# Kernel optimization log

Hardware: AMD Instinct MI355X
Metric: run time of the kernel (lower is better)

## Reference

```python
import jax, jax.numpy as jnp
import numpy as np

B, S, P, D, H = 2, 2048, 2048, 2048, 16
HD = D // H  # head_dim = 128


def setup_inputs() -> dict:
    key = jax.random.key(0)
    ks = jax.random.split(key, 8)
    scale = 1.0 / np.sqrt(D)
    return {
        "x": jax.random.normal(ks[0], (B, S, D), jnp.float32),
        "cache_k": jax.random.normal(ks[1], (B, P, D), jnp.float32),
        "cache_v": jax.random.normal(ks[2], (B, P, D), jnp.float32),
        "wq": jax.random.normal(ks[3], (D, D), jnp.float32) * scale,
        "bq": jnp.zeros((D,), jnp.float32),
        "wk": jax.random.normal(ks[4], (D, D), jnp.float32) * scale,
        "bk": jnp.zeros((D,), jnp.float32),
        "wv": jax.random.normal(ks[5], (D, D), jnp.float32) * scale,
        "bv": jnp.zeros((D,), jnp.float32),
        "wo": jax.random.normal(ks[6], (D, D), jnp.float32) * scale,
        "bo": jnp.zeros((D,), jnp.float32),
    }


def reference(x, cache_k, cache_v, wq, bq, wk, bk, wv, bv, wo, bo):
    bsz, seq_len, _ = x.shape
    q = x @ wq + bq                      # [B,S,D]
    k_new = x @ wk + bk                  # [B,S,D]
    v_new = x @ wv + bv
    # use_cache=True path: prepend cached (detached) keys/values
    k = jnp.concatenate([cache_k, k_new], axis=1)  # [B,P+S,D]
    v = jnp.concatenate([cache_v, v_new], axis=1)
    # split heads: [B,H,S,hd] / [B,H,K,hd]
    q = q.reshape(bsz, seq_len, H, HD).transpose(0, 2, 1, 3)
    k = k.reshape(bsz, -1, H, HD).transpose(0, 2, 1, 3)
    v = v.reshape(bsz, -1, H, HD).transpose(0, 2, 1, 3)
    scores = jnp.einsum("bhsd,bhkd->bhsk", q, k) / jnp.sqrt(jnp.float32(HD))
    attn = jax.nn.softmax(scores, axis=-1)          # full-softmax, no mask
    out = jnp.einsum("bhsk,bhkd->bhsd", attn, v)
    out = out.transpose(0, 2, 1, 3).reshape(bsz, seq_len, D)
    return out @ wo + bo
```

## Files before the change

### kernel.cpp

```cpp
#include <hip/hip_runtime.h>

typedef __attribute__((ext_vector_type(8))) short short8;
typedef __attribute__((ext_vector_type(4))) short short4_;
typedef __attribute__((ext_vector_type(4))) float f32x4;

#define AS1 __attribute__((address_space(1)))
#define AS3 __attribute__((address_space(3)))
#define GLD16(g, l) __builtin_amdgcn_global_load_lds((const AS1 void*)(g), (AS3 void*)(l), 16, 0, 0)

#define C2 0.12751743f

__device__ __forceinline__ unsigned short f2bf(float f) {
  unsigned int u = __float_as_uint(f);
  u += 0x7fffu + ((u >> 16) & 1u);
  return (unsigned short)(u >> 16);
}

__global__ __launch_bounds__(256) void k_transpose_w(
    const float* __restrict__ wq, const float* __restrict__ wk,
    const float* __restrict__ wv, const float* __restrict__ wo,
    unsigned short* __restrict__ wqkvT, unsigned short* __restrict__ woT)
{
  __shared__ float tile[64][65];
  const int z = blockIdx.z;
  const float* src = (z == 0) ? wq : (z == 1) ? wk : (z == 2) ? wv : wo;
  unsigned short* dst = (z == 3) ? woT : (wqkvT + (size_t)z * 2048 * 2048);
  const int k0 = blockIdx.y * 64, n0 = blockIdx.x * 64;
  const int tid = threadIdx.x;
#pragma unroll
  for (int p = 0; p < 4; ++p) {
    const int r = p * 16 + (tid >> 4);
    const int c = (tid & 15) * 4;
    f32x4 v = *(const f32x4*)(src + (size_t)(k0 + r) * 2048 + n0 + c);
    tile[r][c + 0] = v[0]; tile[r][c + 1] = v[1];
    tile[r][c + 2] = v[2]; tile[r][c + 3] = v[3];
  }
  __syncthreads();
#pragma unroll
  for (int p = 0; p < 2; ++p) {
    const int task = tid + p * 256;
    const int n = task >> 3;
    const int kc = (task & 7) * 8;
    short8 ov;
#pragma unroll
    for (int j = 0; j < 8; ++j) ov[j] = (short)f2bf(tile[kc + j][n]);
    *(short8*)(dst + (size_t)(n0 + n) * 2048 + k0 + kc) = ov;
  }
}

__global__ __launch_bounds__(256) void k_convert(
    const float* __restrict__ x, const float* __restrict__ ck, const float* __restrict__ cv,
    unsigned short* __restrict__ xbf, unsigned short* __restrict__ kfull,
    unsigned short* __restrict__ vfull)
{
  const int z = blockIdx.y;
  const size_t idx = ((size_t)blockIdx.x * 256 + threadIdx.x) * 8;
  const float* src = (z == 0) ? x : (z == 1) ? ck : cv;
  f32x4 a = *(const f32x4*)(src + idx);
  f32x4 b = *(const f32x4*)(src + idx + 4);
  short8 ov;
#pragma unroll
  for (int j = 0; j < 4; ++j) { ov[j] = (short)f2bf(a[j]); ov[j + 4] = (short)f2bf(b[j]); }
  unsigned short* dp; size_t di;
  if (z == 0) { dp = xbf; di = idx; }
  else {
    const size_t r = idx >> 11, cl = idx & 2047;
    const size_t orow = r + (r & ~(size_t)2047);
    di = orow * 2048 + cl;
    dp = (z == 1) ? kfull : vfull;
  }
  *(short8*)(dp + di) = ov;
}

template <int MODE>
__global__ __launch_bounds__(256, 2) void k_gemm(
    const unsigned short* __restrict__ A, const unsigned short* __restrict__ BT,
    unsigned short* __restrict__ Oq, unsigned short* __restrict__ Ok,
    unsigned short* __restrict__ Ov, float* __restrict__ Of,
    const float* __restrict__ b0, const float* __restrict__ b1,
    const float* __restrict__ b2, int K)
{
  __shared__ unsigned short Ah[128 * 32];
  __shared__ unsigned short Bh[128 * 32];
  const int tid = threadIdx.x;
  const int l = tid & 63, w = tid >> 6;
  const int l15 = l & 15, g = l >> 4;
  const int wr = (w >> 1) * 64, wc = (w & 1) * 64;
  const int bm = blockIdx.y, bn = blockIdx.x;
  const unsigned short* Ab = A + (size_t)bm * 128 * K;
  const unsigned short* Bb = BT + (size_t)bn * 128 * K;
  const int srow = l >> 2;
  const int scol = (l & 3) * 8;
  f32x4 acc[4][4];
#pragma unroll
  for (int i = 0; i < 4; ++i)
#pragma unroll
    for (int j = 0; j < 4; ++j)
#pragma unroll
      for (int e = 0; e < 4; ++e) acc[i][j][e] = 0.f;

  for (int kt = 0; kt < K; kt += 32) {
#pragma unroll
    for (int cc = 0; cc < 2; ++cc) {
      const int c = w + cc * 4;
      GLD16(Ab + (size_t)(c * 16 + srow) * K + kt + scol, &Ah[c * 512]);
      GLD16(Bb + (size_t)(c * 16 + srow) * K + kt + scol, &Bh[c * 512]);
    }
    __syncthreads();
    short8 af[4], bf[4];
#pragma unroll
    for (int i = 0; i < 4; ++i) {
      af[i] = *(const short8*)&Ah[(wr + i * 16 + l15) * 32 + g * 8];
      bf[i] = *(const short8*)&Bh[(wc + i * 16 + l15) * 32 + g * 8];
    }
#pragma unroll
    for (int i = 0; i < 4; ++i)
#pragma unroll
      for (int j = 0; j < 4; ++j)
        acc[i][j] = __builtin_amdgcn_mfma_f32_16x16x32_bf16(af[i], bf[j], acc[i][j], 0, 0, 0);
    __syncthreads();
  }

  const int rbase = bm * 128 + wr + g * 4;
  if (MODE == 0) {
    const int nglob = bn * 128;
    const int which = nglob >> 11;
    const int ncol0 = nglob & 2047;
    unsigned short* dst = (which == 0) ? Oq : (which == 1) ? Ok : Ov;
    const float* bias = (which == 0) ? b0 : (which == 1) ? b1 : b2;
#pragma unroll
    for (int j = 0; j < 4; ++j) {
      const int cc = ncol0 + wc + j * 16 + l15;
      const float bb = bias[cc];
#pragma unroll
      for (int i = 0; i < 4; ++i) {
#pragma unroll
        for (int ii = 0; ii < 4; ++ii) {
          const int rr = rbase + i * 16 + ii;
          const size_t orow = (which == 0) ? (size_t)rr
                                           : (size_t)(rr + (rr & ~2047) + 2048);
          dst[orow * 2048 + cc] = f2bf(acc[i][j][ii] + bb);
        }
      }
    }
  } else {
#pragma unroll
    for (int j = 0; j < 4; ++j) {
      const int cc = bn * 128 + wc + j * 16 + l15;
      const float bb = b0[cc];
#pragma unroll
      for (int i = 0; i < 4; ++i) {
#pragma unroll
        for (int ii = 0; ii < 4; ++ii) {
          const int rr = rbase + i * 16 + ii;
          Of[(size_t)rr * 2048 + cc] = acc[i][j][ii] + bb;
        }
      }
    }
  }
}

__global__ __launch_bounds__(256, 2) void k_flash(
    const unsigned short* __restrict__ qbuf, const unsigned short* __restrict__ kfull,
    const unsigned short* __restrict__ vfull, unsigned short* __restrict__ attnout)
{
  __shared__ char smem[65536];
  const int tid = threadIdx.x;
  const int l = tid & 63, w = tid >> 6;
  const int l15 = l & 15, g = l >> 4;
  const int qt = blockIdx.x, bh = blockIdx.y;
  const int b = bh >> 4, h = bh & 15;

  short8 qfA[4], qfB[4];
  {
    const int qrowA = qt * 128 + w * 32 + l15;
    const unsigned short* qpA = qbuf + ((size_t)(b * 2048 + qrowA)) * 2048 + h * 128 + g * 8;
    const unsigned short* qpB = qpA + 16 * 2048;
#pragma unroll
    for (int kk = 0; kk < 4; ++kk) {
      qfA[kk] = *(const short8*)(qpA + kk * 32);
      qfB[kk] = *(const short8*)(qpB + kk * 32);
    }
  }
  f32x4 oA[8], oB[8];
#pragma unroll
  for (int d = 0; d < 8; ++d)
#pragma unroll
    for (int e = 0; e < 4; ++e) { oA[d][e] = 0.f; oB[d][e] = 0.f; }
  float mA = -1e30f, mB = -1e30f, lsA = 0.f, lsB = 0.f;

  const unsigned short* kbase = kfull + ((size_t)b * 4096) * 2048 + h * 128;
  const unsigned short* vbase = vfull + ((size_t)b * 4096) * 2048 + h * 128;

  const int vg4 = tid & 15;
  const int vdc = tid >> 4;
  const int vcol4 = (vg4 & 8) | ((vg4 & 3) << 1) | ((vg4 >> 2) & 1);
  const int vu = vcol4 >> 1;
  const int vhalf = (vcol4 & 1) * 8;
  const int ksrow = l >> 4, ksu = l & 15;

  auto STAGEK = [&](int t, char* Kn) {
    const unsigned short* kb = kbase + (size_t)t * 64 * 2048;
#pragma unroll
    for (int ci = 0; ci < 4; ++ci) {
      const int c = w * 4 + ci;
      const int row = c * 4 + ksrow;
      GLD16(kb + (size_t)row * 2048 + ((ksu ^ (row & 7)) * 8), Kn + c * 1024);
    }
  };
  auto VLOAD = [&](int t, short8* r) {
    const unsigned short* vp = vbase + ((size_t)t * 64 + vg4 * 4) * 2048 + vdc * 8;
    r[0] = *(const short8*)(vp);
    r[1] = *(const short8*)(vp + 2048);
    r[2] = *(const short8*)(vp + 4096);
    r[3] = *(const short8*)(vp + 6144);
  };
  auto VWRITE = [&](char* Vn, short8* r) {
#pragma unroll
    for (int d = 0; d < 8; ++d) {
      const int row = vdc * 8 + d;
      const int mm = (d ^ vdc) & 7;
      short4_ pk; pk[0] = r[0][d]; pk[1] = r[1][d]; pk[2] = r[2][d]; pk[3] = r[3][d];
      *(short4_*)(Vn + row * 128 + ((vu ^ mm) * 16) + vhalf) = pk;
    }
  };

  {
    short8 vr[4];
    STAGEK(0, smem);
    VLOAD(0, vr);
    VWRITE(smem + 16384, vr);
    __syncthreads();
  }

  for (int t = 0; t < 64; ++t) {
    char* Kc = smem + (t & 1) * 32768;
    char* Vc = Kc + 16384;
    char* Kn = smem + ((t + 1) & 1) * 32768;
    char* Vn = Kn + 16384;
    const bool pre = (t + 1) < 64;
    short8 vr[4];
    if (pre) {
      STAGEK(t + 1, Kn);
      VLOAD(t + 1, vr);
    }
    f32x4 scA[4], scB[4];
    __builtin_amdgcn_s_setprio(1);
#pragma unroll
    for (int kc = 0; kc < 4; ++kc) {
      f32x4 a0, a1;
#pragma unroll
      for (int e = 0; e < 4; ++e) { a0[e] = 0.f; a1[e] = 0.f; }
      const int rowk = kc * 16 + l15;
      const int mk = rowk & 7;
#pragma unroll
      for (int kk = 0; kk < 4; ++kk) {
        short8 kf = *(const short8*)(Kc + rowk * 256 + (((kk * 4 + g) ^ mk) * 16));
        a0 = __builtin_amdgcn_mfma_f32_16x16x32_bf16(kf, qfA[kk], a0, 0, 0, 0);
        a1 = __builtin_amdgcn_mfma_f32_16x16x32_bf16(kf, qfB[kk], a1, 0, 0, 0);
      }
      scA[kc] = a0; scB[kc] = a1;
    }
    __builtin_amdgcn_s_setprio(0);
    if (pre) VWRITE(Vn, vr);

    short8 pfA[2], pfB[2];
    {
      float tm = fmaxf(fmaxf(scA[0][0], scA[0][1]), fmaxf(scA[0][2], scA[0][3]));
#pragma unroll
      for (int kc = 1; kc < 4; ++kc)
        tm = fmaxf(tm, fmaxf(fmaxf(scA[kc][0], scA[kc][1]), fmaxf(scA[kc][2], scA[kc][3])));
      tm = fmaxf(tm, __shfl_xor(tm, 16, 64));
      tm = fmaxf(tm, __shfl_xor(tm, 32, 64));
      if (!__all(tm <= mA + 16.f)) {
        const float mn = fmaxf(mA, tm);
        const float f = exp2f(C2 * (mA - mn));
        mA = mn; lsA *= f;
#pragma unroll
        for (int d = 0; d < 8; ++d)
#pragma unroll
          for (int e = 0; e < 4; ++e) oA[d][e] *= f;
      }
      const float mc = C2 * mA;
      float ps = 0.f;
#pragma unroll
      for (int c = 0; c < 2; ++c) {
#pragma unroll
        for (int i = 0; i < 4; ++i) {
          const float p0 = exp2f(fmaf(C2, scA[2 * c][i], -mc));
          const float p1 = exp2f(fmaf(C2, scA[2 * c + 1][i], -mc));
          ps += p0 + p1;
          pfA[c][i] = (short)f2bf(p0);
          pfA[c][i + 4] = (short)f2bf(p1);
        }
      }
      ps += __shfl_xor(ps, 16, 64);
      ps += __shfl_xor(ps, 32, 64);
      lsA += ps;
    }
    {
      float tm = fmaxf(fmaxf(scB[0][0], scB[0][1]), fmaxf(scB[0][2], scB[0][3]));
#pragma unroll
      for (int kc = 1; kc < 4; ++kc)
        tm = fmaxf(tm, fmaxf(fmaxf(scB[kc][0], scB[kc][1]), fmaxf(scB[kc][2], scB[kc][3])));
      tm = fmaxf(tm, __shfl_xor(tm, 16, 64));
      tm = fmaxf(tm, __shfl_xor(tm, 32, 64));
      if (!__all(tm <= mB + 16.f)) {
        const float mn = fmaxf(mB, tm);
        const float f = exp2f(C2 * (mB - mn));
        mB = mn; lsB *= f;
#pragma unroll
        for (int d = 0; d < 8; ++d)
#pragma unroll
          for (int e = 0; e < 4; ++e) oB[d][e] *= f;
      }
      const float mc = C2 * mB;
      float ps = 0.f;
#pragma unroll
      for (int c = 0; c < 2; ++c) {
#pragma unroll
        for (int i = 0; i < 4; ++i) {
          const float p0 = exp2f(fmaf(C2, scB[2 * c][i], -mc));
          const float p1 = exp2f(fmaf(C2, scB[2 * c + 1][i], -mc));
          ps += p0 + p1;
          pfB[c][i] = (short)f2bf(p0);
          pfB[c][i + 4] = (short)f2bf(p1);
        }
      }
      ps += __shfl_xor(ps, 16, 64);
      ps += __shfl_xor(ps, 32, 64);
      lsB += ps;
    }

    __builtin_amdgcn_s_setprio(1);
#pragma unroll
    for (int c = 0; c < 2; ++c) {
#pragma unroll
      for (int d = 0; d < 8; ++d) {
        const int rowv = d * 16 + l15;
        const int mv = (rowv ^ (rowv >> 3)) & 7;
        short8 vf = *(const short8*)(Vc + rowv * 128 + ((((c * 4 + g) ^ mv)) * 16));
        oA[d] = __builtin_amdgcn_mfma_f32_16x16x32_bf16(vf, pfA[c], oA[d], 0, 0, 0);
        oB[d] = __builtin_amdgcn_mfma_f32_16x16x32_bf16(vf, pfB[c], oB[d], 0, 0, 0);
      }
    }
    __builtin_amdgcn_s_setprio(0);
    __syncthreads();
  }

  __syncthreads();
  const float invA = 1.0f / lsA, invB = 1.0f / lsB;
  char* ep = smem;
#pragma unroll
  for (int d = 0; d < 8; ++d) {
    short4_ pa, pb;
#pragma unroll
    for (int e = 0; e < 4; ++e) {
      pa[e] = (short)f2bf(oA[d][e] * invA);
      pb[e] = (short)f2bf(oB[d][e] * invB);
    }
    const int colb = (d * 16 + g * 4) * 2;
    *(short4_*)(ep + (w * 32 + l15) * 272 + colb) = pa;
    *(short4_*)(ep + (w * 32 + 16 + l15) * 272 + colb) = pb;
  }
  __syncthreads();
#pragma unroll
  for (int i = 0; i < 8; ++i) {
    const int task = tid + i * 256;
    const int row = task >> 4, un = task & 15;
    short8 ov = *(const short8*)(ep + row * 272 + un * 16);
    const int qg = qt * 128 + row;
    *(short8*)(attnout + ((size_t)(b * 2048 + qg)) * 2048 + h * 128 + un * 8) = ov;
  }
}

extern "C" void kernel_launch(void* const* d_in, const int* in_sizes, int n_in,
                              void* d_out, int out_size, void* d_ws, size_t ws_size,
                              hipStream_t stream)
{
  const float* x  = (const float*)d_in[0];
  const float* ck = (const float*)d_in[1];
  const float* cv = (const float*)d_in[2];
  const float* wq = (const float*)d_in[3];
  const float* bq = (const float*)d_in[4];
  const float* wk = (const float*)d_in[5];
  const float* bk = (const float*)d_in[6];
  const float* wv = (const float*)d_in[7];
  const float* bv = (const float*)d_in[8];
  const float* wo = (const float*)d_in[9];
  const float* bo = (const float*)d_in[10];
  float* out = (float*)d_out;

  char* ws = (char*)d_ws;
  unsigned short* xbf   = (unsigned short*)(ws);
  unsigned short* wqkvT = (unsigned short*)(ws + 16777216ull);
  unsigned short* woT   = (unsigned short*)(ws + 41943040ull);
  unsigned short* qbuf  = (unsigned short*)(ws + 50331648ull);
  unsigned short* kfull = (unsigned short*)(ws + 67108864ull);
  unsigned short* vfull = (unsigned short*)(ws + 100663296ull);
  unsigned short* aout  = (unsigned short*)(ws + 134217728ull);

  k_transpose_w<<<dim3(32, 32, 4), 256, 0, stream>>>(wq, wk, wv, wo, wqkvT, woT);
  k_convert<<<dim3(4096, 3), 256, 0, stream>>>(x, ck, cv, xbf, kfull, vfull);
  k_gemm<0><<<dim3(48, 32), 256, 0, stream>>>(xbf, wqkvT, qbuf, kfull, vfull, nullptr,
                                              bq, bk, bv, 2048);
  k_flash<<<dim3(16, 32), 256, 0, stream>>>(qbuf, kfull, vfull, aout);
  k_gemm<1><<<dim3(16, 32), 256, 0, stream>>>(aout, woT, nullptr, nullptr, nullptr, out,
                                              bo, nullptr, nullptr, 2048);
}
```

Before: 555.7 us.

## Add pipelined 256x256 QKV GEMM, swizzle block order, pack softmax conversions

Replaces the QKV projection GEMM with a 512-thread, 256x256-tile kernel. It uses a 4-slot, 128KB dynamic-LDS ring fed by global_load_lds, a rotated LDS layout to avoid bank conflicts, interleaved half-tile MFMA phases, and a swizzled block-to-tile mapping for L2 locality. The flash kernel gets a swizzled 1D grid order, v_max3 row-max reductions and packed v_cvt_pk_bf16_f32 conversions for P, and its V LDS write is moved after the softmax. The output GEMM is split into its own non-templated kernel. The risks are lower occupancy from the large LDS footprint and only 384 blocks for the QKV GEMM. The packed conversion may round differently from the manual f2bf.

```diff
diff --git a/kernel.cpp b/kernel.cpp
--- a/kernel.cpp
+++ b/kernel.cpp
@@ -3,6 +3,7 @@
 typedef __attribute__((ext_vector_type(8))) short short8;
 typedef __attribute__((ext_vector_type(4))) short short4_;
 typedef __attribute__((ext_vector_type(4))) float f32x4;
+typedef __attribute__((ext_vector_type(4))) unsigned int u32x4;
 
 #define AS1 __attribute__((address_space(1)))
 #define AS3 __attribute__((address_space(3)))
@@ -14,6 +15,16 @@
   unsigned int u = __float_as_uint(f);
   u += 0x7fffu + ((u >> 16) & 1u);
   return (unsigned short)(u >> 16);
+}
+__device__ __forceinline__ unsigned int cvtpk(float a, float b) {
+  unsigned int r;
+  asm("v_cvt_pk_bf16_f32 %0, %1, %2" : "=v"(r) : "v"(a), "v"(b));
+  return r;
+}
+__device__ __forceinline__ float max3f(float a, float b, float c) {
+  float r;
+  asm("v_max3_f32 %0, %1, %2, %3" : "=v"(r) : "v"(a), "v"(b), "v"(c));
+  return r;
 }
 
 __global__ __launch_bounds__(256) void k_transpose_w(
@@ -72,13 +83,125 @@
   *(short8*)(dp + di) = ov;
 }
 
-template <int MODE>
-__global__ __launch_bounds__(256, 2) void k_gemm(
+__global__ __launch_bounds__(512, 2) void k_gemm8(
     const unsigned short* __restrict__ A, const unsigned short* __restrict__ BT,
     unsigned short* __restrict__ Oq, unsigned short* __restrict__ Ok,
-    unsigned short* __restrict__ Ov, float* __restrict__ Of,
+    unsigned short* __restrict__ Ov,
     const float* __restrict__ b0, const float* __restrict__ b1,
-    const float* __restrict__ b2, int K)
+    const float* __restrict__ b2)
+{
+  extern __shared__ char lds[];
+  char* ABase = lds;
+  char* BBase = lds + 65536;
+  const int tid = threadIdx.x;
+  const int l = tid & 63, w = tid >> 6;
+  const int l15 = l & 15, g = l >> 4;
+  const int wr = w >> 2, wc = w & 3;
+  const int bid = blockIdx.x;
+  const int sw = (bid & 7) * 48 + (bid >> 3);
+  const int bm = sw / 24, bn = sw % 24;
+
+  const unsigned short* Ab = A + (size_t)bm * 256 * 2048;
+  const unsigned short* Bb = BT + (size_t)bn * 256 * 2048;
+  const int sr = l >> 2;
+  const int su = l & 3;
+
+  f32x4 acc[8][4];
+#pragma unroll
+  for (int i = 0; i < 8; ++i)
+#pragma unroll
+    for (int j = 0; j < 4; ++j)
+#pragma unroll
+      for (int e = 0; e < 4; ++e) acc[i][j][e] = 0.f;
+
+  auto STAGE = [&](const unsigned short* src, char* base, int slot, int tt) {
+    char* dst = base + slot * 16384 + w * 2048;
+#pragma unroll
+    for (int i = 0; i < 2; ++i) {
+      const int row = w * 32 + i * 16 + sr;
+      const int gu = (su - (row >> 1)) & 3;
+      GLD16(src + (size_t)row * 2048 + tt * 32 + gu * 8, dst + i * 1024);
+    }
+  };
+
+  STAGE(Ab, ABase, 0, 0); STAGE(Bb, BBase, 0, 0);
+  STAGE(Ab, ABase, 1, 1); STAGE(Bb, BBase, 1, 1);
+  asm volatile("s_waitcnt vmcnt(4)" ::: "memory");
+  __builtin_amdgcn_sched_barrier(0);
+  __builtin_amdgcn_s_barrier();
+
+  for (int t = 0; t < 64; ++t) {
+    const char* Ac = ABase + (t & 3) * 16384;
+    const char* Bc = BBase + (t & 3) * 16384;
+    const int t2 = (t + 2 < 64) ? t + 2 : 0;
+    const int s2 = (t + 2) & 3;
+    short8 av[4], bv[4];
+#pragma unroll
+    for (int mf = 0; mf < 4; ++mf) {
+      const int ar = wr * 128 + mf * 16 + l15;
+      av[mf] = *(const short8*)(Ac + ar * 64 + (((g + (ar >> 1)) & 3) * 16));
+    }
+#pragma unroll
+    for (int nf = 0; nf < 4; ++nf) {
+      const int br = wc * 64 + nf * 16 + l15;
+      bv[nf] = *(const short8*)(Bc + br * 64 + (((g + (br >> 1)) & 3) * 16));
+    }
+    STAGE(Ab, ABase, s2, t2);
+    __builtin_amdgcn_s_barrier();
+    asm volatile("s_waitcnt lgkmcnt(0)" ::: "memory");
+    __builtin_amdgcn_sched_barrier(0);
+    __builtin_amdgcn_s_setprio(1);
+#pragma unroll
+    for (int mf = 0; mf < 4; ++mf)
+#pragma unroll
+      for (int nf = 0; nf < 4; ++nf)
+        acc[mf][nf] = __builtin_amdgcn_mfma_f32_16x16x32_bf16(av[mf], bv[nf], acc[mf][nf], 0, 0, 0);
+    __builtin_amdgcn_s_setprio(0);
+    __builtin_amdgcn_s_barrier();
+#pragma unroll
+    for (int mf = 0; mf < 4; ++mf) {
+      const int ar = wr * 128 + (mf + 4) * 16 + l15;
+      av[mf] = *(const short8*)(Ac + ar * 64 + (((g + (ar >> 1)) & 3) * 16));
+    }
+    STAGE(Bb, BBase, s2, t2);
+    __builtin_amdgcn_s_barrier();
+    asm volatile("s_waitcnt lgkmcnt(0)" ::: "memory");
+    __builtin_amdgcn_sched_barrier(0);
+    __builtin_amdgcn_s_setprio(1);
+#pragma unroll
+    for (int mf = 0; mf < 4; ++mf)
+#pragma unroll
+      for (int nf = 0; nf < 4; ++nf)
+        acc[mf + 4][nf] = __builtin_amdgcn_mfma_f32_16x16x32_bf16(av[mf], bv[nf], acc[mf + 4][nf], 0, 0, 0);
+    __builtin_amdgcn_s_setprio(0);
+    asm volatile("s_waitcnt vmcnt(4)" ::: "memory");
+    __builtin_amdgcn_sched_barrier(0);
+    __builtin_amdgcn_s_barrier();
+  }
+
+  const int nglob0 = bn * 256;
+  const int nsec = nglob0 >> 11;
+  unsigned short* dst = (nsec == 0) ? Oq : (nsec == 1) ? Ok : Ov;
+  const float* bias = (nsec == 0) ? b0 : (nsec == 1) ? b1 : b2;
+#pragma unroll
+  for (int nf = 0; nf < 4; ++nf) {
+    const int cc = (nglob0 & 2047) + wc * 64 + nf * 16 + l15;
+    const float bb = bias[cc];
+#pragma unroll
+    for (int mf = 0; mf < 8; ++mf) {
+#pragma unroll
+      for (int ii = 0; ii < 4; ++ii) {
+        const int rr = bm * 256 + wr * 128 + mf * 16 + g * 4 + ii;
+        const size_t orow = (nsec == 0) ? (size_t)rr : (size_t)(rr + (rr & ~2047) + 2048);
+        dst[orow * 2048 + cc] = f2bf(acc[mf][nf][ii] + bb);
+      }
+    }
+  }
+}
+
+__global__ __launch_bounds__(256, 2) void k_gemmo(
+    const unsigned short* __restrict__ A, const unsigned short* __restrict__ BT,
+    float* __restrict__ Of, const float* __restrict__ b0, int K)
 {
   __shared__ unsigned short Ah[128 * 32];
   __shared__ unsigned short Bh[128 * 32];
@@ -120,41 +243,16 @@
         acc[i][j] = __builtin_amdgcn_mfma_f32_16x16x32_bf16(af[i], bf[j], acc[i][j], 0, 0, 0);
     __syncthreads();
   }
-
-  const int rbase = bm * 128 + wr + g * 4;
-  if (MODE == 0) {
-    const int nglob = bn * 128;
-    const int which = nglob >> 11;
-    const int ncol0 = nglob & 2047;
-    unsigned short* dst = (which == 0) ? Oq : (which == 1) ? Ok : Ov;
-    const float* bias = (which == 0) ? b0 : (which == 1) ? b1 : b2;
-#pragma unroll
-    for (int j = 0; j < 4; ++j) {
-      const int cc = ncol0 + wc + j * 16 + l15;
-      const float bb = bias[cc];
-#pragma unroll
-      for (int i = 0; i < 4; ++i) {
-#pragma unroll
-        for (int ii = 0; ii < 4; ++ii) {
-          const int rr = rbase + i * 16 + ii;
-          const size_t orow = (which == 0) ? (size_t)rr
-                                           : (size_t)(rr + (rr & ~2047) + 2048);
-          dst[orow * 2048 + cc] = f2bf(acc[i][j][ii] + bb);
-        }
-      }
-    }
-  } else {
-#pragma unroll
-    for (int j = 0; j < 4; ++j) {
-      const int cc = bn * 128 + wc + j * 16 + l15;
-      const float bb = b0[cc];
-#pragma unroll
-      for (int i = 0; i < 4; ++i) {
-#pragma unroll
-        for (int ii = 0; ii < 4; ++ii) {
-          const int rr = rbase + i * 16 + ii;
-          Of[(size_t)rr * 2048 + cc] = acc[i][j][ii] + bb;
-        }
+#pragma unroll
+  for (int j = 0; j < 4; ++j) {
+    const int cc = bn * 128 + wc + j * 16 + l15;
+    const float bb = b0[cc];
+#pragma unroll
+    for (int i = 0; i < 4; ++i) {
+#pragma unroll
+      for (int ii = 0; ii < 4; ++ii) {
+        const int rr = bm * 128 + wr + g * 4 + i * 16 + ii;
+        Of[(size_t)rr * 2048 + cc] = acc[i][j][ii] + bb;
       }
     }
   }
@@ -168,7 +266,9 @@
   const int tid = threadIdx.x;
   const int l = tid & 63, w = tid >> 6;
   const int l15 = l & 15, g = l >> 4;
-  const int qt = blockIdx.x, bh = blockIdx.y;
+  const int bid = blockIdx.x;
+  const int sw = (bid & 7) * 64 + (bid >> 3);
+  const int qt = sw & 15, bh = sw >> 4;
   const int b = bh >> 4, h = bh & 15;
 
   short8 qfA[4], qfB[4];
@@ -262,14 +362,17 @@
       scA[kc] = a0; scB[kc] = a1;
     }
     __builtin_amdgcn_s_setprio(0);
-    if (pre) VWRITE(Vn, vr);
 
     short8 pfA[2], pfB[2];
     {
-      float tm = fmaxf(fmaxf(scA[0][0], scA[0][1]), fmaxf(scA[0][2], scA[0][3]));
-#pragma unroll
-      for (int kc = 1; kc < 4; ++kc)
-        tm = fmaxf(tm, fmaxf(fmaxf(scA[kc][0], scA[kc][1]), fmaxf(scA[kc][2], scA[kc][3])));
+      float tm = max3f(scA[0][0], scA[0][1], scA[0][2]);
+      tm = max3f(tm, scA[0][3], scA[1][0]);
+      tm = max3f(tm, scA[1][1], scA[1][2]);
+      tm = max3f(tm, scA[1][3], scA[2][0]);
+      tm = max3f(tm, scA[2][1], scA[2][2]);
+      tm = max3f(tm, scA[2][3], scA[3][0]);
+      tm = max3f(tm, scA[3][1], scA[3][2]);
+      tm = fmaxf(tm, scA[3][3]);
       tm = fmaxf(tm, __shfl_xor(tm, 16, 64));
       tm = fmaxf(tm, __shfl_xor(tm, 32, 64));
       if (!__all(tm <= mA + 16.f)) {
@@ -282,27 +385,36 @@
           for (int e = 0; e < 4; ++e) oA[d][e] *= f;
       }
       const float mc = C2 * mA;
-      float ps = 0.f;
-#pragma unroll
-      for (int c = 0; c < 2; ++c) {
+      float p[4][4];
+      float ps0 = 0.f, ps1 = 0.f;
+#pragma unroll
+      for (int kc = 0; kc < 4; ++kc) {
 #pragma unroll
         for (int i = 0; i < 4; ++i) {
-          const float p0 = exp2f(fmaf(C2, scA[2 * c][i], -mc));
-          const float p1 = exp2f(fmaf(C2, scA[2 * c + 1][i], -mc));
-          ps += p0 + p1;
-          pfA[c][i] = (short)f2bf(p0);
-          pfA[c][i + 4] = (short)f2bf(p1);
+          p[kc][i] = exp2f(fmaf(C2, scA[kc][i], -mc));
+          if (i & 1) ps1 += p[kc][i]; else ps0 += p[kc][i];
         }
       }
+      float ps = ps0 + ps1;
       ps += __shfl_xor(ps, 16, 64);
       ps += __shfl_xor(ps, 32, 64);
       lsA += ps;
+      u32x4 q0 = { cvtpk(p[0][0], p[0][1]), cvtpk(p[0][2], p[0][3]),
+                   cvtpk(p[1][0], p[1][1]), cvtpk(p[1][2], p[1][3]) };
+      u32x4 q1 = { cvtpk(p[2][0], p[2][1]), cvtpk(p[2][2], p[2][3]),
+                   cvtpk(p[3][0], p[3][1]), cvtpk(p[3][2], p[3][3]) };
+      pfA[0] = __builtin_bit_cast(short8, q0);
+      pfA[1] = __builtin_bit_cast(short8, q1);
     }
     {
-      float tm = fmaxf(fmaxf(scB[0][0], scB[0][1]), fmaxf(scB[0][2], scB[0][3]));
-#pragma unroll
-      for (int kc = 1; kc < 4; ++kc)
-        tm = fmaxf(tm, fmaxf(fmaxf(scB[kc][0], scB[kc][1]), fmaxf(scB[kc][2], scB[kc][3])));
+      float tm = max3f(scB[0][0], scB[0][1], scB[0][2]);
+      tm = max3f(tm, scB[0][3], scB[1][0]);
+      tm = max3f(tm, scB[1][1], scB[1][2]);
+      tm = max3f(tm, scB[1][3], scB[2][0]);
+      tm = max3f(tm, scB[2][1], scB[2][2]);
+      tm = max3f(tm, scB[2][3], scB[3][0]);
+      tm = max3f(tm, scB[3][1], scB[3][2]);
+      tm = fmaxf(tm, scB[3][3]);
       tm = fmaxf(tm, __shfl_xor(tm, 16, 64));
       tm = fmaxf(tm, __shfl_xor(tm, 32, 64));
       if (!__all(tm <= mB + 16.f)) {
@@ -315,22 +427,29 @@
           for (int e = 0; e < 4; ++e) oB[d][e] *= f;
       }
       const float mc = C2 * mB;
-      float ps = 0.f;
-#pragma unroll
-      for (int c = 0; c < 2; ++c) {
+      float p[4][4];
+      float ps0 = 0.f, ps1 = 0.f;
+#pragma unroll
+      for (int kc = 0; kc < 4; ++kc) {
 #pragma unroll
         for (int i = 0; i < 4; ++i) {
-          const float p0 = exp2f(fmaf(C2, scB[2 * c][i], -mc));
-          const float p1 = exp2f(fmaf(C2, scB[2 * c + 1][i], -mc));
-          ps += p0 + p1;
-          pfB[c][i] = (short)f2bf(p0);
-          pfB[c][i + 4] = (short)f2bf(p1);
+          p[kc][i] = exp2f(fmaf(C2, scB[kc][i], -mc));
+          if (i & 1) ps1 += p[kc][i]; else ps0 += p[kc][i];
         }
       }
+      float ps = ps0 + ps1;
       ps += __shfl_xor(ps, 16, 64);
       ps += __shfl_xor(ps, 32, 64);
       lsB += ps;
-    }
+      u32x4 q0 = { cvtpk(p[0][0], p[0][1]), cvtpk(p[0][2], p[0][3]),
+                   cvtpk(p[1][0], p[1][1]), cvtpk(p[1][2], p[1][3]) };
+      u32x4 q1 = { cvtpk(p[2][0], p[2][1]), cvtpk(p[2][2], p[2][3]),
+                   cvtpk(p[3][0], p[3][1]), cvtpk(p[3][2], p[3][3]) };
+      pfB[0] = __builtin_bit_cast(short8, q0);
+      pfB[1] = __builtin_bit_cast(short8, q1);
+    }
+
+    if (pre) VWRITE(Vn, vr);
 
     __builtin_amdgcn_s_setprio(1);
 #pragma unroll
@@ -400,11 +519,12 @@
   unsigned short* vfull = (unsigned short*)(ws + 100663296ull);
   unsigned short* aout  = (unsigned short*)(ws + 134217728ull);
 
+  (void)hipFuncSetAttribute((const void*)k_gemm8,
+                            hipFuncAttributeMaxDynamicSharedMemorySize, 131072);
+
   k_transpose_w<<<dim3(32, 32, 4), 256, 0, stream>>>(wq, wk, wv, wo, wqkvT, woT);
   k_convert<<<dim3(4096, 3), 256, 0, stream>>>(x, ck, cv, xbf, kfull, vfull);
-  k_gemm<0><<<dim3(48, 32), 256, 0, stream>>>(xbf, wqkvT, qbuf, kfull, vfull, nullptr,
-                                              bq, bk, bv, 2048);
-  k_flash<<<dim3(16, 32), 256, 0, stream>>>(qbuf, kfull, vfull, aout);
-  k_gemm<1><<<dim3(16, 32), 256, 0, stream>>>(aout, woT, nullptr, nullptr, nullptr, out,
-                                              bo, nullptr, nullptr, 2048);
-}
+  k_gemm8<<<dim3(384), 512, 131072, stream>>>(xbf, wqkvT, qbuf, kfull, vfull, bq, bk, bv);
+  k_flash<<<dim3(512), 256, 0, stream>>>(qbuf, kfull, vfull, aout);
+  k_gemmo<<<dim3(16, 32), 256, 0, stream>>>(aout, woT, out, bo, 2048);
+}
```

New measurement: 560.2 us. About the same (+0.8%).
